# Optimization experiments

Measured on AMD Instinct MI355X. Metric: run time of the kernel, lower is better.

## Reference

```python
import jax, jax.numpy as jnp
import numpy as np
from math import sqrt

# Complete K-ary tree: level l has K**l nodes; children of node j at level l
# are nodes j*K .. j*K+K-1 of level l+1. Levels are processed leaves->root.
K = 4
LEVELS = 9
N_NODES = (K ** LEVELS - 1) // (K - 1)  # 87381
X_SIZE = 256
H_SIZE = 256
A_SIZE = 256
N_HEADS = 8
A_K = A_SIZE // N_HEADS


def setup_inputs() -> dict:
    key = jax.random.key(0)
    ks = jax.random.split(key, 20)
    s = 0.02
    d = {
        'x': jax.random.normal(ks[0], (N_NODES, X_SIZE), dtype=jnp.float32),
        'W_iou': jax.random.normal(ks[1], (X_SIZE, 3 * H_SIZE), dtype=jnp.float32) * s,
        'b_iou': jnp.zeros((3 * H_SIZE,), dtype=jnp.float32),
        'W_f': jax.random.normal(ks[2], (X_SIZE, H_SIZE), dtype=jnp.float32) * s,
        'b_f': jnp.zeros((H_SIZE,), dtype=jnp.float32),
        'Wq': jax.random.normal(ks[3], (X_SIZE, A_SIZE), dtype=jnp.float32) * s,
        'bq': jax.random.normal(ks[4], (A_SIZE,), dtype=jnp.float32) * s,
        'Wk': jax.random.normal(ks[5], (H_SIZE, A_SIZE), dtype=jnp.float32) * s,
        'bk': jax.random.normal(ks[6], (A_SIZE,), dtype=jnp.float32) * s,
        'Wv': jax.random.normal(ks[7], (H_SIZE, A_SIZE), dtype=jnp.float32) * s,
        'bv': jax.random.normal(ks[8], (A_SIZE,), dtype=jnp.float32) * s,
        'Wl': jax.random.normal(ks[9], (A_SIZE, A_SIZE), dtype=jnp.float32) * s,
        'bl': jax.random.normal(ks[10], (A_SIZE,), dtype=jnp.float32) * s,
        'Uiou_w': jax.random.normal(ks[11], (A_SIZE, 3 * H_SIZE), dtype=jnp.float32) * s,
        'Uiou_b': jax.random.normal(ks[12], (3 * H_SIZE,), dtype=jnp.float32) * s,
        'Uf_w': jax.random.normal(ks[13], (A_SIZE, H_SIZE), dtype=jnp.float32) * s,
        'Uf_b': jax.random.normal(ks[14], (H_SIZE,), dtype=jnp.float32) * s,
    }
    return d


def _tree_lstm(x, W_iou, b_iou, W_f, b_f, Wq, bq, Wk, bk, Wv, bv, Wl, bl,
               Uiou_w, Uiou_b, Uf_w, Uf_b):
    scale = 1.0 / sqrt(A_K)
    x_iou = x @ W_iou + b_iou          # [N, 3H]
    x_f = x @ W_f + b_f                # [N, H]
    starts = [(K ** l - 1) // (K - 1) for l in range(LEVELS)]
    h_lvl = [None] * LEVELS
    c_lvl = [None] * LEVELS
    for l in reversed(range(LEVELS)):
        s0 = starts[l]
        n = K ** l
        xi = x_iou[s0:s0 + n]
        xf = x_f[s0:s0 + n]
        if l == LEVELS - 1:  # leaves: empty mailbox
            iou = xi
            fc_sum = jnp.zeros((n, H_SIZE), dtype=x.dtype)
        else:
            ch_h = h_lvl[l + 1].reshape(n, K, H_SIZE)  # children mailbox 'h'
            ch_c = c_lvl[l + 1].reshape(n, K, H_SIZE)  # children mailbox 'c'
            q = (x[s0:s0 + n] @ Wq + bq).reshape(n, N_HEADS, A_K)
            kk = (ch_h @ Wk + bk).reshape(n, K, N_HEADS, A_K)
            vv = (ch_h @ Wv + bv).reshape(n, K, N_HEADS, A_K)
            logits = jnp.einsum('nhd,nkhd->nhk', q, kk) * scale
            attn = jax.nn.softmax(logits, axis=-1)
            out = jnp.einsum('nhk,nkhd->nhd', attn, vv).reshape(n, A_SIZE)
            h_attn = out @ Wl + bl
            h_iou = h_attn @ Uiou_w + Uiou_b
            h_f = h_attn @ Uf_w + Uf_b
            f = jax.nn.sigmoid(xf + h_f)[:, None, :]   # same f for all children
            fc_sum = jnp.sum(ch_c * f, axis=1)
            iou = xi + h_iou
        i, o, u = jnp.split(iou, 3, axis=1)
        c_new = jax.nn.sigmoid(i) * jnp.tanh(u) + fc_sum
        h_new = jax.nn.sigmoid(o) * jnp.tanh(c_new)
        h_lvl[l] = h_new
        c_lvl[l] = c_new
    h = jnp.concatenate(h_lvl, axis=0)
    c = jnp.concatenate(c_lvl, axis=0)
    return h, c


def reference(x, W_iou, b_iou, W_f, b_f, Wq, bq, Wk, bk, Wv, bv, Wl, bl,
              Uiou_w, Uiou_b, Uf_w, Uf_b):
    return _tree_lstm(x, W_iou, b_iou, W_f, b_f, Wq, bq, Wk, bk, Wv, bv,
                      Wl, bl, Uiou_w, Uiou_b, Uf_w, Uf_b)
```

## Files before the change

### kernel.cpp

```cpp
#include <hip/hip_runtime.h>
#include <hip/hip_bf16.h>
#include <math.h>

constexpr int LEVELS_ = 9;
constexpr int N_NODES_ = 87381;
constexpr int HS = 256;
constexpr int N_HEADS_ = 8;

typedef __attribute__((ext_vector_type(8))) short bf16x8;
typedef __attribute__((ext_vector_type(4))) float f32x4;
typedef __attribute__((ext_vector_type(4))) float float4v;

__device__ __forceinline__ short f2bf(float f) {
    union { float f; unsigned u; } a; a.f = f;
    unsigned r = (a.u + 0x7fff + ((a.u >> 16) & 1)) >> 16;
    return (short)r;
}
__device__ __forceinline__ float bf2f(short s) {
    union { unsigned u; float f; } a; a.u = ((unsigned)(unsigned short)s) << 16;
    return a.f;
}
__device__ __forceinline__ float sigm(float x) { return 1.f / (1.f + expf(-x)); }

__device__ __forceinline__ void gl_lds16(const short* g, short* l) {
    __builtin_amdgcn_global_load_lds(
        (const __attribute__((address_space(1))) void*)g,
        (__attribute__((address_space(3))) void*)l, 16, 0, 0);
}

__global__ __launch_bounds__(256) void gemm_bf16(
    const short* __restrict__ A, const short* __restrict__ Bt,
    const float* __restrict__ bias, const short* __restrict__ Cadd,
    void* __restrict__ Cout, int M, int N, int Kd, int out_bf16)
{
    __shared__ short smem[2 * 128 * 64];
    short* As = smem;
    short* Bs = smem + 128 * 64;

    const int tid = threadIdx.x;
    const int lane = tid & 63;
    const int w = tid >> 6;
    const int row0 = blockIdx.y * 128;
    const int col0 = blockIdx.x * 128;
    const int wm = (w >> 1) * 64;
    const int wn = (w & 1) * 64;
    const int q = lane >> 4;
    const int mr = lane & 15;

    const int srl = lane >> 3;
    const int scs = ((lane & 7) ^ srl) * 8;

    f32x4 acc[4][4];
    #pragma unroll
    for (int i = 0; i < 4; i++)
        #pragma unroll
        for (int j = 0; j < 4; j++) acc[i][j] = (f32x4){0.f, 0.f, 0.f, 0.f};

    for (int k0 = 0; k0 < Kd; k0 += 64) {
        __syncthreads();
        #pragma unroll
        for (int i = 0; i < 4; ++i) {
            int s = w * 4 + i;
            int r = s * 8 + srl;
            gl_lds16(A + (size_t)(row0 + r) * Kd + k0 + scs, As + s * 512);
            gl_lds16(Bt + (size_t)(col0 + r) * Kd + k0 + scs, Bs + s * 512);
        }
        __syncthreads();
        #pragma unroll
        for (int h = 0; h < 2; ++h) {
            bf16x8 af[4], bfr[4];
            #pragma unroll
            for (int i = 0; i < 4; ++i) {
                int r = wm + i * 16 + mr;
                af[i] = *(const bf16x8*)(As + r * 64 + ((h * 4 + q) ^ (mr & 7)) * 8);
            }
            #pragma unroll
            for (int j = 0; j < 4; ++j) {
                int r = wn + j * 16 + mr;
                bfr[j] = *(const bf16x8*)(Bs + r * 64 + ((h * 4 + q) ^ (mr & 7)) * 8);
            }
            #pragma unroll
            for (int i = 0; i < 4; ++i)
                #pragma unroll
                for (int j = 0; j < 4; ++j)
                    acc[i][j] = __builtin_amdgcn_mfma_f32_16x16x32_bf16(
                        af[i], bfr[j], acc[i][j], 0, 0, 0);
        }
    }

    if (out_bf16) {
        __syncthreads();
        short* Cs = smem;
        #pragma unroll
        for (int j = 0; j < 4; ++j) {
            int col = wn + j * 16 + mr;
            float bv = bias ? bias[col0 + col] : 0.f;
            #pragma unroll
            for (int i = 0; i < 4; ++i) {
                #pragma unroll
                for (int r = 0; r < 4; ++r) {
                    int lr = wm + i * 16 + q * 4 + r;
                    float v = acc[i][j][r] + bv;
                    if (Cadd && row0 + lr < M)
                        v += bf2f(Cadd[(size_t)(row0 + lr) * N + col0 + col]);
                    Cs[lr * 128 + col] = f2bf(v);
                }
            }
        }
        __syncthreads();
        #pragma unroll
        for (int i = 0; i < 8; ++i) {
            int chunk = i * 256 + tid;
            int lr = chunk >> 4;
            int c8 = (chunk & 15) * 8;
            if (row0 + lr < M)
                *(bf16x8*)((short*)Cout + (size_t)(row0 + lr) * N + col0 + c8) =
                    *(const bf16x8*)(Cs + lr * 128 + c8);
        }
    } else {
        #pragma unroll
        for (int j = 0; j < 4; ++j) {
            int col = col0 + wn + j * 16 + mr;
            float bv = bias ? bias[col] : 0.f;
            #pragma unroll
            for (int i = 0; i < 4; ++i) {
                #pragma unroll
                for (int r = 0; r < 4; ++r) {
                    int grow = row0 + wm + i * 16 + q * 4 + r;
                    if (grow < M) {
                        size_t off = (size_t)grow * N + col;
                        float v = acc[i][j][r] + bv;
                        if (Cadd) v += bf2f(Cadd[off]);
                        ((float*)Cout)[off] = v;
                    }
                }
            }
        }
    }
}

__global__ __launch_bounds__(256) void attn_kernel(
    const short* __restrict__ Q, const short* __restrict__ KV,
    short* __restrict__ Ob, int n)
{
    int t = blockIdx.x * 256 + threadIdx.x;
    int pair = t >> 5;
    int lane = t & 31;
    if (pair >= n * N_HEADS_) return;
    int node = pair >> 3;
    int head = pair & 7;
    const float scale = 0.17677669529663687f;

    int qoff = node * HS + head * 32 + lane;
    float qv = bf2f(Q[qoff]);

    float logit[4];
    #pragma unroll
    for (int c = 0; c < 4; c++) {
        float p = qv * bf2f(KV[(size_t)(4 * node + c) * 512 + head * 32 + lane]);
        #pragma unroll
        for (int off = 16; off >= 1; off >>= 1)
            p += __shfl_xor(p, off, 32);
        logit[c] = p * scale;
    }
    float m = fmaxf(fmaxf(logit[0], logit[1]), fmaxf(logit[2], logit[3]));
    float e[4], s = 0.f;
    #pragma unroll
    for (int c = 0; c < 4; c++) { e[c] = expf(logit[c] - m); s += e[c]; }
    float inv = 1.f / s;
    float o = 0.f;
    #pragma unroll
    for (int c = 0; c < 4; c++)
        o += (e[c] * inv) * bf2f(KV[(size_t)(4 * node + c) * 512 + 256 + head * 32 + lane]);
    Ob[qoff] = f2bf(o);
}

__global__ __launch_bounds__(256) void cell_internal(
    const short* __restrict__ iouf, const float* __restrict__ c_child,
    float* __restrict__ h_out, float* __restrict__ c_out,
    short* __restrict__ hb_out, int n)
{
    int t = blockIdx.x * 256 + threadIdx.x;
    if (t >= n * 32) return;
    int node = t >> 5;
    int j8 = (t & 31) * 8;
    size_t base = (size_t)node * 1024;
    bf16x8 vi = *(const bf16x8*)(iouf + base + j8);
    bf16x8 vo = *(const bf16x8*)(iouf + base + 256 + j8);
    bf16x8 vu = *(const bf16x8*)(iouf + base + 512 + j8);
    bf16x8 vf = *(const bf16x8*)(iouf + base + 768 + j8);
    float4v cc[4][2];
    #pragma unroll
    for (int c = 0; c < 4; ++c) {
        const float* cp = c_child + (size_t)(4 * node + c) * 256 + j8;
        cc[c][0] = *(const float4v*)cp;
        cc[c][1] = *(const float4v*)(cp + 4);
    }
    float4v hv[2], cv[2];
    bf16x8 hbv;
    #pragma unroll
    for (int e = 0; e < 8; ++e) {
        float fv = sigm(bf2f(vf[e]));
        float csum = cc[0][e >> 2][e & 3] + cc[1][e >> 2][e & 3] +
                     cc[2][e >> 2][e & 3] + cc[3][e >> 2][e & 3];
        float cn = sigm(bf2f(vi[e])) * tanhf(bf2f(vu[e])) + csum * fv;
        float hn = sigm(bf2f(vo[e])) * tanhf(cn);
        hv[e >> 2][e & 3] = hn;
        cv[e >> 2][e & 3] = cn;
        hbv[e] = f2bf(hn);
    }
    size_t o = (size_t)t * 8;
    *(float4v*)(h_out + o) = hv[0]; *(float4v*)(h_out + o + 4) = hv[1];
    *(float4v*)(c_out + o) = cv[0]; *(float4v*)(c_out + o + 4) = cv[1];
    *(bf16x8*)(hb_out + o) = hbv;
}

__global__ __launch_bounds__(256) void cell_leaf(
    const short* __restrict__ iou,
    float* __restrict__ h_out, float* __restrict__ c_out,
    short* __restrict__ hb_out, int n)
{
    int t = blockIdx.x * 256 + threadIdx.x;
    if (t >= n * 32) return;
    int node = t >> 5;
    int j8 = (t & 31) * 8;
    size_t base = (size_t)node * 768;
    bf16x8 vi = *(const bf16x8*)(iou + base + j8);
    bf16x8 vo = *(const bf16x8*)(iou + base + 256 + j8);
    bf16x8 vu = *(const bf16x8*)(iou + base + 512 + j8);
    float4v hv[2], cv[2];
    bf16x8 hbv;
    #pragma unroll
    for (int e = 0; e < 8; ++e) {
        float cn = sigm(bf2f(vi[e])) * tanhf(bf2f(vu[e]));
        float hn = sigm(bf2f(vo[e])) * tanhf(cn);
        hv[e >> 2][e & 3] = hn;
        cv[e >> 2][e & 3] = cn;
        hbv[e] = f2bf(hn);
    }
    size_t o = (size_t)t * 8;
    *(float4v*)(h_out + o) = hv[0]; *(float4v*)(h_out + o + 4) = hv[1];
    *(float4v*)(c_out + o) = cv[0]; *(float4v*)(c_out + o + 4) = cv[1];
    *(bf16x8*)(hb_out + o) = hbv;
}

__global__ __launch_bounds__(256) void level_fused(
    const short* __restrict__ hb, const float* __restrict__ c_all,
    const short* __restrict__ qb, const short* __restrict__ xi,
    const short* __restrict__ B3t, const short* __restrict__ Wlt,
    const short* __restrict__ Bt2,
    const float* __restrict__ bias_kv, const float* __restrict__ bl,
    const float* __restrict__ biasU,
    float* __restrict__ h_all, float* __restrict__ c_out_g,
    short* __restrict__ hb_out, int s0, int sc, int n)
{
    __shared__ __align__(16) char smem[50176];
    short* sh_h    = (short*)smem;
    short* sh_kv   = (short*)(smem + 16896);
    short* sh_out  = (short*)smem;
    short* sh_ha   = (short*)(smem + 8448);
    float* sh_iouf = (float*)(smem + 16896);

    const int tid = threadIdx.x;
    const int lane = tid & 63;
    const int w = tid >> 6;
    const int q = lane >> 4;
    const int mr = lane & 15;
    const int p0 = blockIdx.x * 8;
    const int np = (n - p0 < 8) ? (n - p0) : 8;
    const int nch = 4 * np;

    #pragma unroll
    for (int i = 0; i < 4; ++i) {
        int chunk = i * 256 + tid;
        int r = chunk >> 5;
        int c8 = (chunk & 31) * 8;
        bf16x8 v = {};
        if (r < nch) v = *(const bf16x8*)(hb + (size_t)(sc + 4 * p0 + r) * 256 + c8);
        *(bf16x8*)(sh_h + r * 264 + c8) = v;
    }
    __syncthreads();

    {
        f32x4 acc[2][8];
        #pragma unroll
        for (int rt = 0; rt < 2; ++rt)
            #pragma unroll
            for (int ct = 0; ct < 8; ++ct) acc[rt][ct] = (f32x4){0.f, 0.f, 0.f, 0.f};
        #pragma unroll 1
        for (int k0 = 0; k0 < 256; k0 += 32) {
            bf16x8 a0 = *(const bf16x8*)(sh_h + mr * 264 + k0 + q * 8);
            bf16x8 a1 = *(const bf16x8*)(sh_h + (16 + mr) * 264 + k0 + q * 8);
            #pragma unroll
            for (int ct = 0; ct < 8; ++ct) {
                int col = w * 128 + ct * 16 + mr;
                bf16x8 b = *(const bf16x8*)(B3t + (size_t)col * 256 + k0 + q * 8);
                acc[0][ct] = __builtin_amdgcn_mfma_f32_16x16x32_bf16(a0, b, acc[0][ct], 0, 0, 0);
                acc[1][ct] = __builtin_amdgcn_mfma_f32_16x16x32_bf16(a1, b, acc[1][ct], 0, 0, 0);
            }
        }
        #pragma unroll
        for (int ct = 0; ct < 8; ++ct) {
            int col = w * 128 + ct * 16 + mr;
            float bv = bias_kv[col];
            #pragma unroll
            for (int rt = 0; rt < 2; ++rt)
                #pragma unroll
                for (int r = 0; r < 4; ++r) {
                    int row = rt * 16 + q * 4 + r;
                    sh_kv[row * 520 + col] = f2bf(acc[rt][ct][r] + bv);
                }
        }
    }
    __syncthreads();

    {
        const int grp0 = tid >> 5;
        const int l32 = tid & 31;
        #pragma unroll 1
        for (int it = 0; it < 8; ++it) {
            int grp = it * 8 + grp0;
            int node = grp >> 3, head = grp & 7;
            if (node < np) {
                float qv = bf2f(qb[(size_t)(s0 + p0 + node) * 256 + head * 32 + l32]);
                float logit[4];
                #pragma unroll
                for (int c = 0; c < 4; ++c) {
                    float p = qv * bf2f(sh_kv[(4 * node + c) * 520 + head * 32 + l32]);
                    #pragma unroll
                    for (int off = 16; off >= 1; off >>= 1)
                        p += __shfl_xor(p, off, 32);
                    logit[c] = p * 0.17677669529663687f;
                }
                float mx = fmaxf(fmaxf(logit[0], logit[1]), fmaxf(logit[2], logit[3]));
                float e[4], s = 0.f;
                #pragma unroll
                for (int c = 0; c < 4; ++c) { e[c] = expf(logit[c] - mx); s += e[c]; }
                float inv = 1.f / s;
                float o = 0.f;
                #pragma unroll
                for (int c = 0; c < 4; ++c)
                    o += (e[c] * inv) * bf2f(sh_kv[(4 * node + c) * 520 + 256 + head * 32 + l32]);
                sh_out[node * 264 + head * 32 + l32] = f2bf(o);
            }
        }
    }
    __syncthreads();

    {
        f32x4 acc[4];
        #pragma unroll
        for (int ct = 0; ct < 4; ++ct) acc[ct] = (f32x4){0.f, 0.f, 0.f, 0.f};
        #pragma unroll 1
        for (int k0 = 0; k0 < 256; k0 += 32) {
            bf16x8 a = *(const bf16x8*)(sh_out + mr * 264 + k0 + q * 8);
            #pragma unroll
            for (int ct = 0; ct < 4; ++ct) {
                int col = w * 64 + ct * 16 + mr;
                bf16x8 b = *(const bf16x8*)(Wlt + (size_t)col * 256 + k0 + q * 8);
                acc[ct] = __builtin_amdgcn_mfma_f32_16x16x32_bf16(a, b, acc[ct], 0, 0, 0);
            }
        }
        #pragma unroll
        for (int ct = 0; ct < 4; ++ct) {
            int col = w * 64 + ct * 16 + mr;
            float bv = bl[col];
            #pragma unroll
            for (int r = 0; r < 4; ++r) {
                int row = q * 4 + r;
                if (row < np) sh_ha[row * 264 + col] = f2bf(acc[ct][r] + bv);
            }
        }
    }
    __syncthreads();

    {
        f32x4 acc[16];
        #pragma unroll
        for (int ct = 0; ct < 16; ++ct) acc[ct] = (f32x4){0.f, 0.f, 0.f, 0.f};
        #pragma unroll 1
        for (int k0 = 0; k0 < 256; k0 += 32) {
            bf16x8 a = *(const bf16x8*)(sh_ha + mr * 264 + k0 + q * 8);
            #pragma unroll
            for (int ct = 0; ct < 16; ++ct) {
                int col = w * 256 + ct * 16 + mr;
                bf16x8 b = *(const bf16x8*)(Bt2 + (size_t)col * 256 + k0 + q * 8);
                acc[ct] = __builtin_amdgcn_mfma_f32_16x16x32_bf16(a, b, acc[ct], 0, 0, 0);
            }
        }
        __syncthreads();
        #pragma unroll
        for (int ct = 0; ct < 16; ++ct) {
            int col = w * 256 + ct * 16 + mr;
            float bU = biasU[col];
            #pragma unroll
            for (int r = 0; r < 4; ++r) {
                int row = q * 4 + r;
                if (row < np)
                    sh_iouf[row * 1024 + col] =
                        acc[ct][r] + bU + bf2f(xi[(size_t)(s0 + p0 + row) * 1024 + col]);
            }
        }
    }
    __syncthreads();

    #pragma unroll 1
    for (int it = 0; it < 8; ++it) {
        int t = it * 256 + tid;
        if (t < np * 256) {
            int node = t >> 8, j = t & 255;
            float iv = sh_iouf[node * 1024 + j];
            float ov = sh_iouf[node * 1024 + 256 + j];
            float uv = sh_iouf[node * 1024 + 512 + j];
            float fv = sigm(sh_iouf[node * 1024 + 768 + j]);
            float fc = 0.f;
            #pragma unroll
            for (int c = 0; c < 4; ++c)
                fc += c_all[(size_t)(sc + 4 * (p0 + node) + c) * 256 + j] * fv;
            float cn = sigm(iv) * tanhf(uv) + fc;
            float hn = sigm(ov) * tanhf(cn);
            size_t o = (size_t)(s0 + p0 + node) * 256 + j;
            h_all[o] = hn;
            c_out_g[o] = cn;
            hb_out[o] = f2bf(hn);
        }
    }
}

__global__ __launch_bounds__(256) void conv_x(
    const float* __restrict__ x, short* __restrict__ xb, int n8)
{
    int t = blockIdx.x * 256 + threadIdx.x;
    if (t >= n8) return;
    float4v a = *(const float4v*)(x + (size_t)t * 8);
    float4v b = *(const float4v*)(x + (size_t)t * 8 + 4);
    bf16x8 o;
    o[0] = f2bf(a.x); o[1] = f2bf(a.y); o[2] = f2bf(a.z); o[3] = f2bf(a.w);
    o[4] = f2bf(b.x); o[5] = f2bf(b.y); o[6] = f2bf(b.z); o[7] = f2bf(b.w);
    *(bf16x8*)(xb + (size_t)t * 8) = o;
}

__global__ __launch_bounds__(256) void prep_weights(
    const float* __restrict__ W_iou, const float* __restrict__ W_f,
    const float* __restrict__ Uiou_w, const float* __restrict__ Uf_w,
    const float* __restrict__ Wk, const float* __restrict__ Wv,
    const float* __restrict__ Wq, const float* __restrict__ Wl,
    const float* __restrict__ b_iou, const float* __restrict__ b_f,
    const float* __restrict__ Uiou_b, const float* __restrict__ Uf_b,
    const float* __restrict__ bk, const float* __restrict__ bv,
    short* __restrict__ Bt1, short* __restrict__ Bt2, short* __restrict__ B3t,
    short* __restrict__ Wqt, short* __restrict__ Wlt,
    float* __restrict__ biasX, float* __restrict__ biasU,
    float* __restrict__ bias_kv)
{
    int t = blockIdx.x * 256 + threadIdx.x;
    if (t < 262144) {
        int nn = t >> 8, k = t & 255;
        float v = (nn < 768) ? W_iou[k * 768 + nn] : W_f[k * 256 + (nn - 768)];
        Bt1[t] = f2bf(v);
        return;
    }
    t -= 262144;
    if (t < 262144) {
        int nn = t >> 8, k = t & 255;
        float v = (nn < 768) ? Uiou_w[k * 768 + nn] : Uf_w[k * 256 + (nn - 768)];
        Bt2[t] = f2bf(v);
        return;
    }
    t -= 262144;
    if (t < 131072) {
        int nn = t >> 8, k = t & 255;
        float v = (nn < 256) ? Wk[k * 256 + nn] : Wv[k * 256 + (nn - 256)];
        B3t[t] = f2bf(v);
        return;
    }
    t -= 131072;
    if (t < 65536) { int nn = t >> 8, k = t & 255; Wqt[t] = f2bf(Wq[k * 256 + nn]); return; }
    t -= 65536;
    if (t < 65536) { int nn = t >> 8, k = t & 255; Wlt[t] = f2bf(Wl[k * 256 + nn]); return; }
    t -= 65536;
    if (t < 1024) { biasX[t] = (t < 768) ? b_iou[t] : b_f[t - 768]; return; }
    t -= 1024;
    if (t < 1024) { biasU[t] = (t < 768) ? Uiou_b[t] : Uf_b[t - 768]; return; }
    t -= 1024;
    if (t < 512) { bias_kv[t] = (t < 256) ? bk[t] : bv[t - 256]; return; }
}

static inline void launch_gemm(const short* A, const short* Bt, const float* bias,
                               const short* Cadd, void* C, int M, int N, int Kd,
                               int out_bf16, hipStream_t stream)
{
    dim3 grid(N / 128, (M + 127) / 128);
    gemm_bf16<<<grid, 256, 0, stream>>>(A, Bt, bias, Cadd, C, M, N, Kd, out_bf16);
}

extern "C" void kernel_launch(void* const* d_in, const int* in_sizes, int n_in,
                              void* d_out, int out_size, void* d_ws, size_t ws_size,
                              hipStream_t stream)
{
    const float* x      = (const float*)d_in[0];
    const float* W_iou  = (const float*)d_in[1];
    const float* b_iou  = (const float*)d_in[2];
    const float* W_f    = (const float*)d_in[3];
    const float* b_f    = (const float*)d_in[4];
    const float* Wq     = (const float*)d_in[5];
    const float* bq     = (const float*)d_in[6];
    const float* Wk     = (const float*)d_in[7];
    const float* bk     = (const float*)d_in[8];
    const float* Wv     = (const float*)d_in[9];
    const float* bv     = (const float*)d_in[10];
    const float* Wl     = (const float*)d_in[11];
    const float* bl     = (const float*)d_in[12];
    const float* Uiou_w = (const float*)d_in[13];
    const float* Uiou_b = (const float*)d_in[14];
    const float* Uf_w   = (const float*)d_in[15];
    const float* Uf_b   = (const float*)d_in[16];

    float* h_all = (float*)d_out;
    float* c_all = h_all + (size_t)N_NODES_ * HS;

    char* p = (char*)d_ws;
    short* xb   = (short*)p; p += (size_t)N_NODES_ * 256 * 2;
    short* hb   = (short*)p; p += (size_t)N_NODES_ * 256 * 2;
    short* xl   = (short*)p; p += (size_t)65536 * 768 * 2;
    short* xi   = (short*)p; p += (size_t)21845 * 1024 * 2;
    short* qb   = (short*)p; p += (size_t)21845 * 256 * 2;
    short* KVb  = (short*)p; p += (size_t)65536 * 512 * 2;
    short* outb = (short*)p; p += (size_t)16384 * 256 * 2;
    short* hab  = (short*)p; p += (size_t)16384 * 256 * 2;
    short* ioufb= (short*)p; p += (size_t)16384 * 1024 * 2;
    short* Bt1  = (short*)p; p += (size_t)1024 * 256 * 2;
    short* Bt2  = (short*)p; p += (size_t)1024 * 256 * 2;
    short* B3t  = (short*)p; p += (size_t)512 * 256 * 2;
    short* Wqt  = (short*)p; p += (size_t)256 * 256 * 2;
    short* Wlt  = (short*)p; p += (size_t)256 * 256 * 2;
    float* biasX   = (float*)p; p += 1024 * 4;
    float* biasU   = (float*)p; p += 1024 * 4;
    float* bias_kv = (float*)p; p += 512 * 4;

    static const int starts[LEVELS_] = {0, 1, 5, 21, 85, 341, 1365, 5461, 21845};

    {
        int n8 = N_NODES_ * 256 / 8;
        conv_x<<<(n8 + 255) / 256, 256, 0, stream>>>(x, xb, n8);
        int total = 262144 + 262144 + 131072 + 65536 + 65536 + 1024 + 1024 + 512;
        prep_weights<<<(total + 255) / 256, 256, 0, stream>>>(
            W_iou, W_f, Uiou_w, Uf_w, Wk, Wv, Wq, Wl,
            b_iou, b_f, Uiou_b, Uf_b, bk, bv,
            Bt1, Bt2, B3t, Wqt, Wlt, biasX, biasU, bias_kv);
    }

    launch_gemm(xb + (size_t)21845 * 256, Bt1, biasX, nullptr, xl,
                65536, 768, 256, 1, stream);
    launch_gemm(xb, Bt1, biasX, nullptr, xi, 21845, 1024, 256, 1, stream);
    launch_gemm(xb, Wqt, bq, nullptr, qb, 21845, 256, 256, 1, stream);

    {
        int total = 65536 * 32;
        cell_leaf<<<(total + 255) / 256, 256, 0, stream>>>(
            xl, h_all + (size_t)21845 * HS, c_all + (size_t)21845 * HS,
            hb + (size_t)21845 * HS, 65536);
    }

    for (int l = 7; l >= 6; l--) {
        int n  = 1 << (2 * l);
        int s0 = starts[l];
        int sc = starts[l + 1];
        int nc = 4 * n;

        launch_gemm(hb + (size_t)sc * 256, B3t, bias_kv, nullptr, KVb,
                    nc, 512, 256, 1, stream);
        int pairs = n * N_HEADS_;
        attn_kernel<<<(pairs * 32 + 255) / 256, 256, 0, stream>>>(
            qb + (size_t)s0 * 256, KVb, outb, n);
        launch_gemm(outb, Wlt, bl, nullptr, hab, n, 256, 256, 1, stream);
        launch_gemm(hab, Bt2, biasU, xi + (size_t)s0 * 1024, ioufb,
                    n, 1024, 256, 1, stream);
        int total = n * 32;
        cell_internal<<<(total + 255) / 256, 256, 0, stream>>>(
            ioufb, c_all + (size_t)sc * HS,
            h_all + (size_t)s0 * HS, c_all + (size_t)s0 * HS,
            hb + (size_t)s0 * HS, n);
    }

    for (int l = 5; l >= 0; l--) {
        int n  = 1 << (2 * l);
        int s0 = starts[l];
        int sc = starts[l + 1];
        int blocks = (n + 7) / 8;
        level_fused<<<blocks, 256, 0, stream>>>(
            hb, c_all, qb, xi, B3t, Wlt, Bt2, bias_kv, bl, biasU,
            h_all, c_all, hb, s0, sc, n);
    }
}
```

Before: 935.0 us.

## Fuse LSTM cell into gate GEMM epilogues and KV projection with attention

Weight columns are reordered so that each 128-wide GEMM tile holds the i/o/u/f gates for 32 hidden units, and K/V are interleaved per head. That lets the leaf and internal-level GEMMs apply the LSTM cell in their epilogue, and lets the KV projection kernel run the per-head attention directly from shared memory. The large intermediate buffers (leaf iou, KV, iouf) and their round trips through global memory are removed, along with several kernel launches. In exchange the code adds LDS staging and epilogue work, and the level_fused indexing must agree with the new interleaved layout.

```diff
diff --git a/kernel.cpp b/kernel.cpp
--- a/kernel.cpp
+++ b/kernel.cpp
@@ -27,13 +27,14 @@
         (const __attribute__((address_space(1))) void*)g,
         (__attribute__((address_space(3))) void*)l, 16, 0, 0);
 }
+
 
 __global__ __launch_bounds__(256) void gemm_bf16(
     const short* __restrict__ A, const short* __restrict__ Bt,
     const float* __restrict__ bias, const short* __restrict__ Cadd,
     void* __restrict__ Cout, int M, int N, int Kd, int out_bf16)
 {
-    __shared__ short smem[2 * 128 * 64];
+    __shared__ __align__(16) short smem[2 * 128 * 64];
     short* As = smem;
     short* Bs = smem + 128 * 64;
 
@@ -139,109 +140,246 @@
     }
 }
 
-__global__ __launch_bounds__(256) void attn_kernel(
-    const short* __restrict__ Q, const short* __restrict__ KV,
-    short* __restrict__ Ob, int n)
+__global__ __launch_bounds__(256) void gemm_cell(
+    const short* __restrict__ A, const short* __restrict__ Bt,
+    const float* __restrict__ bias, const short* __restrict__ Cadd,
+    const float* __restrict__ c_child,
+    float* __restrict__ h_out, float* __restrict__ c_out,
+    short* __restrict__ hb_out, int M)
 {
-    int t = blockIdx.x * 256 + threadIdx.x;
-    int pair = t >> 5;
-    int lane = t & 31;
-    if (pair >= n * N_HEADS_) return;
-    int node = pair >> 3;
-    int head = pair & 7;
-    const float scale = 0.17677669529663687f;
-
-    int qoff = node * HS + head * 32 + lane;
-    float qv = bf2f(Q[qoff]);
-
-    float logit[4];
+    __shared__ __align__(16) short smem[128 * 136];
+    short* As = smem;
+    short* Bs = smem + 128 * 64;
+
+    const int tid = threadIdx.x;
+    const int lane = tid & 63;
+    const int w = tid >> 6;
+    const int row0 = blockIdx.y * 128;
+    const int col0 = blockIdx.x * 128;
+    const int wm = (w >> 1) * 64;
+    const int wn = (w & 1) * 64;
+    const int q = lane >> 4;
+    const int mr = lane & 15;
+
+    const int srl = lane >> 3;
+    const int scs = ((lane & 7) ^ srl) * 8;
+
+    f32x4 acc[4][4];
     #pragma unroll
-    for (int c = 0; c < 4; c++) {
-        float p = qv * bf2f(KV[(size_t)(4 * node + c) * 512 + head * 32 + lane]);
-        #pragma unroll
-        for (int off = 16; off >= 1; off >>= 1)
-            p += __shfl_xor(p, off, 32);
-        logit[c] = p * scale;
-    }
-    float m = fmaxf(fmaxf(logit[0], logit[1]), fmaxf(logit[2], logit[3]));
-    float e[4], s = 0.f;
+    for (int i = 0; i < 4; i++)
+        #pragma unroll
+        for (int j = 0; j < 4; j++) acc[i][j] = (f32x4){0.f, 0.f, 0.f, 0.f};
+
+    for (int k0 = 0; k0 < 256; k0 += 64) {
+        __syncthreads();
+        #pragma unroll
+        for (int i = 0; i < 4; ++i) {
+            int s = w * 4 + i;
+            int r = s * 8 + srl;
+            gl_lds16(A + (size_t)(row0 + r) * 256 + k0 + scs, As + s * 512);
+            gl_lds16(Bt + (size_t)(col0 + r) * 256 + k0 + scs, Bs + s * 512);
+        }
+        __syncthreads();
+        #pragma unroll
+        for (int h = 0; h < 2; ++h) {
+            bf16x8 af[4], bfr[4];
+            #pragma unroll
+            for (int i = 0; i < 4; ++i) {
+                int r = wm + i * 16 + mr;
+                af[i] = *(const bf16x8*)(As + r * 64 + ((h * 4 + q) ^ (mr & 7)) * 8);
+            }
+            #pragma unroll
+            for (int j = 0; j < 4; ++j) {
+                int r = wn + j * 16 + mr;
+                bfr[j] = *(const bf16x8*)(Bs + r * 64 + ((h * 4 + q) ^ (mr & 7)) * 8);
+            }
+            #pragma unroll
+            for (int i = 0; i < 4; ++i)
+                #pragma unroll
+                for (int j = 0; j < 4; ++j)
+                    acc[i][j] = __builtin_amdgcn_mfma_f32_16x16x32_bf16(
+                        af[i], bfr[j], acc[i][j], 0, 0, 0);
+        }
+    }
+
+    __syncthreads();
+    short* Cs = smem;
     #pragma unroll
-    for (int c = 0; c < 4; c++) { e[c] = expf(logit[c] - m); s += e[c]; }
-    float inv = 1.f / s;
-    float o = 0.f;
+    for (int j = 0; j < 4; ++j) {
+        int col = wn + j * 16 + mr;
+        float bv = bias[col0 + col];
+        #pragma unroll
+        for (int i = 0; i < 4; ++i) {
+            #pragma unroll
+            for (int r = 0; r < 4; ++r) {
+                int lr = wm + i * 16 + q * 4 + r;
+                float v = acc[i][j][r] + bv;
+                if (Cadd && row0 + lr < M)
+                    v += bf2f(Cadd[(size_t)(row0 + lr) * 1024 + col0 + col]);
+                Cs[lr * 136 + col] = f2bf(v);
+            }
+        }
+    }
+    __syncthreads();
+
+    const int hd0 = blockIdx.x * 32;
+    #pragma unroll 1
+    for (int it = 0; it < 2; ++it) {
+        int chunk = it * 256 + tid;
+        int row = chunk >> 2;
+        int d8 = (chunk & 3) * 8;
+        int gp = row0 + row;
+        if (gp < M) {
+            bf16x8 vi = *(const bf16x8*)(Cs + row * 136 + d8);
+            bf16x8 vo = *(const bf16x8*)(Cs + row * 136 + 32 + d8);
+            bf16x8 vu = *(const bf16x8*)(Cs + row * 136 + 64 + d8);
+            float fc[8] = {0.f, 0.f, 0.f, 0.f, 0.f, 0.f, 0.f, 0.f};
+            if (c_child) {
+                bf16x8 vf = *(const bf16x8*)(Cs + row * 136 + 96 + d8);
+                #pragma unroll
+                for (int c = 0; c < 4; ++c) {
+                    const float* cp = c_child + (size_t)(4 * gp + c) * 256 + hd0 + d8;
+                    float4v a = *(const float4v*)cp;
+                    float4v b = *(const float4v*)(cp + 4);
+                    #pragma unroll
+                    for (int e = 0; e < 4; ++e) { fc[e] += a[e]; fc[4 + e] += b[e]; }
+                }
+                #pragma unroll
+                for (int e = 0; e < 8; ++e) fc[e] *= sigm(bf2f(vf[e]));
+            }
+            float4v hv[2], cv[2];
+            bf16x8 hbv;
+            #pragma unroll
+            for (int e = 0; e < 8; ++e) {
+                float cn = sigm(bf2f(vi[e])) * tanhf(bf2f(vu[e])) + fc[e];
+                float hn = sigm(bf2f(vo[e])) * tanhf(cn);
+                hv[e >> 2][e & 3] = hn;
+                cv[e >> 2][e & 3] = cn;
+                hbv[e] = f2bf(hn);
+            }
+            size_t o = (size_t)gp * 256 + hd0 + d8;
+            *(float4v*)(h_out + o) = hv[0]; *(float4v*)(h_out + o + 4) = hv[1];
+            *(float4v*)(c_out + o) = cv[0]; *(float4v*)(c_out + o + 4) = cv[1];
+            *(bf16x8*)(hb_out + o) = hbv;
+        }
+    }
+}
+
+__global__ __launch_bounds__(256) void kv_attn(
+    const short* __restrict__ A,
+    const short* __restrict__ B3t,
+    const float* __restrict__ bias_kv,
+    const short* __restrict__ qb_lvl,
+    short* __restrict__ outb)
+{
+    __shared__ __align__(16) short smem[2 * 128 * 64 + 32 * 64];
+    short* As = smem;
+    short* Bs = smem + 128 * 64;
+    short* sh_o = smem + 2 * 128 * 64;
+
+    const int tid = threadIdx.x;
+    const int lane = tid & 63;
+    const int w = tid >> 6;
+    const int row0 = blockIdx.y * 128;
+    const int colb = blockIdx.x;
+    const int col0 = colb * 128;
+    const int wm = (w >> 1) * 64;
+    const int wn = (w & 1) * 64;
+    const int q = lane >> 4;
+    const int mr = lane & 15;
+
+    const int srl = lane >> 3;
+    const int scs = ((lane & 7) ^ srl) * 8;
+
+    f32x4 acc[4][4];
     #pragma unroll
-    for (int c = 0; c < 4; c++)
-        o += (e[c] * inv) * bf2f(KV[(size_t)(4 * node + c) * 512 + 256 + head * 32 + lane]);
-    Ob[qoff] = f2bf(o);
-}
-
-__global__ __launch_bounds__(256) void cell_internal(
-    const short* __restrict__ iouf, const float* __restrict__ c_child,
-    float* __restrict__ h_out, float* __restrict__ c_out,
-    short* __restrict__ hb_out, int n)
-{
-    int t = blockIdx.x * 256 + threadIdx.x;
-    if (t >= n * 32) return;
-    int node = t >> 5;
-    int j8 = (t & 31) * 8;
-    size_t base = (size_t)node * 1024;
-    bf16x8 vi = *(const bf16x8*)(iouf + base + j8);
-    bf16x8 vo = *(const bf16x8*)(iouf + base + 256 + j8);
-    bf16x8 vu = *(const bf16x8*)(iouf + base + 512 + j8);
-    bf16x8 vf = *(const bf16x8*)(iouf + base + 768 + j8);
-    float4v cc[4][2];
+    for (int i = 0; i < 4; i++)
+        #pragma unroll
+        for (int j = 0; j < 4; j++) acc[i][j] = (f32x4){0.f, 0.f, 0.f, 0.f};
+
+    for (int k0 = 0; k0 < 256; k0 += 64) {
+        __syncthreads();
+        #pragma unroll
+        for (int i = 0; i < 4; ++i) {
+            int s = w * 4 + i;
+            int r = s * 8 + srl;
+            gl_lds16(A + (size_t)(row0 + r) * 256 + k0 + scs, As + s * 512);
+            gl_lds16(B3t + (size_t)(col0 + r) * 256 + k0 + scs, Bs + s * 512);
+        }
+        __syncthreads();
+        #pragma unroll
+        for (int h = 0; h < 2; ++h) {
+            bf16x8 af[4], bfr[4];
+            #pragma unroll
+            for (int i = 0; i < 4; ++i) {
+                int r = wm + i * 16 + mr;
+                af[i] = *(const bf16x8*)(As + r * 64 + ((h * 4 + q) ^ (mr & 7)) * 8);
+            }
+            #pragma unroll
+            for (int j = 0; j < 4; ++j) {
+                int r = wn + j * 16 + mr;
+                bfr[j] = *(const bf16x8*)(Bs + r * 64 + ((h * 4 + q) ^ (mr & 7)) * 8);
+            }
+            #pragma unroll
+            for (int i = 0; i < 4; ++i)
+                #pragma unroll
+                for (int j = 0; j < 4; ++j)
+                    acc[i][j] = __builtin_amdgcn_mfma_f32_16x16x32_bf16(
+                        af[i], bfr[j], acc[i][j], 0, 0, 0);
+        }
+    }
+
+    __syncthreads();
+    short* Cs = smem;
     #pragma unroll
-    for (int c = 0; c < 4; ++c) {
-        const float* cp = c_child + (size_t)(4 * node + c) * 256 + j8;
-        cc[c][0] = *(const float4v*)cp;
-        cc[c][1] = *(const float4v*)(cp + 4);
-    }
-    float4v hv[2], cv[2];
-    bf16x8 hbv;
-    #pragma unroll
-    for (int e = 0; e < 8; ++e) {
-        float fv = sigm(bf2f(vf[e]));
-        float csum = cc[0][e >> 2][e & 3] + cc[1][e >> 2][e & 3] +
-                     cc[2][e >> 2][e & 3] + cc[3][e >> 2][e & 3];
-        float cn = sigm(bf2f(vi[e])) * tanhf(bf2f(vu[e])) + csum * fv;
-        float hn = sigm(bf2f(vo[e])) * tanhf(cn);
-        hv[e >> 2][e & 3] = hn;
-        cv[e >> 2][e & 3] = cn;
-        hbv[e] = f2bf(hn);
-    }
-    size_t o = (size_t)t * 8;
-    *(float4v*)(h_out + o) = hv[0]; *(float4v*)(h_out + o + 4) = hv[1];
-    *(float4v*)(c_out + o) = cv[0]; *(float4v*)(c_out + o + 4) = cv[1];
-    *(bf16x8*)(hb_out + o) = hbv;
-}
-
-__global__ __launch_bounds__(256) void cell_leaf(
-    const short* __restrict__ iou,
-    float* __restrict__ h_out, float* __restrict__ c_out,
-    short* __restrict__ hb_out, int n)
-{
-    int t = blockIdx.x * 256 + threadIdx.x;
-    if (t >= n * 32) return;
-    int node = t >> 5;
-    int j8 = (t & 31) * 8;
-    size_t base = (size_t)node * 768;
-    bf16x8 vi = *(const bf16x8*)(iou + base + j8);
-    bf16x8 vo = *(const bf16x8*)(iou + base + 256 + j8);
-    bf16x8 vu = *(const bf16x8*)(iou + base + 512 + j8);
-    float4v hv[2], cv[2];
-    bf16x8 hbv;
-    #pragma unroll
-    for (int e = 0; e < 8; ++e) {
-        float cn = sigm(bf2f(vi[e])) * tanhf(bf2f(vu[e]));
-        float hn = sigm(bf2f(vo[e])) * tanhf(cn);
-        hv[e >> 2][e & 3] = hn;
-        cv[e >> 2][e & 3] = cn;
-        hbv[e] = f2bf(hn);
-    }
-    size_t o = (size_t)t * 8;
-    *(float4v*)(h_out + o) = hv[0]; *(float4v*)(h_out + o + 4) = hv[1];
-    *(float4v*)(c_out + o) = cv[0]; *(float4v*)(c_out + o + 4) = cv[1];
-    *(bf16x8*)(hb_out + o) = hbv;
+    for (int j = 0; j < 4; ++j) {
+        int col = wn + j * 16 + mr;
+        float bv = bias_kv[col0 + col];
+        #pragma unroll
+        for (int i = 0; i < 4; ++i) {
+            #pragma unroll
+            for (int r = 0; r < 4; ++r) {
+                int lr = wm + i * 16 + q * 4 + r;
+                Cs[lr * 128 + col] = f2bf(acc[i][j][r] + bv);
+            }
+        }
+    }
+    __syncthreads();
+
+    const int p0 = blockIdx.y * 32;
+    const int grp0 = tid >> 5;
+    const int l32 = tid & 31;
+    #pragma unroll 1
+    for (int it = 0; it < 8; ++it) {
+        int pair = it * 8 + grp0;
+        int pl = pair >> 1, hh = pair & 1;
+        float qv = bf2f(qb_lvl[(size_t)(p0 + pl) * 256 + (colb * 2 + hh) * 32 + l32]);
+        float logit[4];
+        #pragma unroll
+        for (int c = 0; c < 4; ++c) {
+            float pch = qv * bf2f(Cs[(4 * pl + c) * 128 + hh * 64 + l32]);
+            #pragma unroll
+            for (int off = 16; off >= 1; off >>= 1)
+                pch += __shfl_xor(pch, off, 32);
+            logit[c] = pch * 0.17677669529663687f;
+        }
+        float mx = fmaxf(fmaxf(logit[0], logit[1]), fmaxf(logit[2], logit[3]));
+        float e[4], s = 0.f;
+        #pragma unroll
+        for (int c = 0; c < 4; ++c) { e[c] = expf(logit[c] - mx); s += e[c]; }
+        float inv = 1.f / s;
+        float o = 0.f;
+        #pragma unroll
+        for (int c = 0; c < 4; ++c)
+            o += (e[c] * inv) * bf2f(Cs[(4 * pl + c) * 128 + hh * 64 + 32 + l32]);
+        sh_o[pl * 64 + hh * 32 + l32] = f2bf(o);
+    }
+    __syncthreads();
+    {
+        int r = tid >> 3, c8 = (tid & 7) * 8;
+        *(bf16x8*)(outb + (size_t)(p0 + r) * 256 + colb * 64 + c8) =
+            *(const bf16x8*)(sh_o + r * 64 + c8);
+    }
 }
 
 __global__ __launch_bounds__(256) void level_fused(
@@ -326,7 +464,7 @@
                 float logit[4];
                 #pragma unroll
                 for (int c = 0; c < 4; ++c) {
-                    float p = qv * bf2f(sh_kv[(4 * node + c) * 520 + head * 32 + l32]);
+                    float p = qv * bf2f(sh_kv[(4 * node + c) * 520 + head * 64 + l32]);
                     #pragma unroll
                     for (int off = 16; off >= 1; off >>= 1)
                         p += __shfl_xor(p, off, 32);
@@ -340,7 +478,7 @@
                 float o = 0.f;
                 #pragma unroll
                 for (int c = 0; c < 4; ++c)
-                    o += (e[c] * inv) * bf2f(sh_kv[(4 * node + c) * 520 + 256 + head * 32 + l32]);
+                    o += (e[c] * inv) * bf2f(sh_kv[(4 * node + c) * 520 + head * 64 + 32 + l32]);
                 sh_out[node * 264 + head * 32 + l32] = f2bf(o);
             }
         }
@@ -409,10 +547,11 @@
         int t = it * 256 + tid;
         if (t < np * 256) {
             int node = t >> 8, j = t & 255;
-            float iv = sh_iouf[node * 1024 + j];
-            float ov = sh_iouf[node * 1024 + 256 + j];
-            float uv = sh_iouf[node * 1024 + 512 + j];
-            float fv = sigm(sh_iouf[node * 1024 + 768 + j]);
+            int gcol = (j >> 5) * 128 + (j & 31);
+            float iv = sh_iouf[node * 1024 + gcol];
+            float ov = sh_iouf[node * 1024 + gcol + 32];
+            float uv = sh_iouf[node * 1024 + gcol + 64];
+            float fv = sigm(sh_iouf[node * 1024 + gcol + 96]);
             float fc = 0.f;
             #pragma unroll
             for (int c = 0; c < 4; ++c)
@@ -455,22 +594,25 @@
 {
     int t = blockIdx.x * 256 + threadIdx.x;
     if (t < 262144) {
-        int nn = t >> 8, k = t & 255;
-        float v = (nn < 768) ? W_iou[k * 768 + nn] : W_f[k * 256 + (nn - 768)];
+        int gc = t >> 8, k = t & 255;
+        int within = gc & 127, gate = within >> 5, d = (gc >> 7) * 32 + (within & 31);
+        float v = (gate < 3) ? W_iou[k * 768 + gate * 256 + d] : W_f[k * 256 + d];
         Bt1[t] = f2bf(v);
         return;
     }
     t -= 262144;
     if (t < 262144) {
-        int nn = t >> 8, k = t & 255;
-        float v = (nn < 768) ? Uiou_w[k * 768 + nn] : Uf_w[k * 256 + (nn - 768)];
+        int gc = t >> 8, k = t & 255;
+        int within = gc & 127, gate = within >> 5, d = (gc >> 7) * 32 + (within & 31);
+        float v = (gate < 3) ? Uiou_w[k * 768 + gate * 256 + d] : Uf_w[k * 256 + d];
         Bt2[t] = f2bf(v);
         return;
     }
     t -= 262144;
     if (t < 131072) {
-        int nn = t >> 8, k = t & 255;
-        float v = (nn < 256) ? Wk[k * 256 + nn] : Wv[k * 256 + (nn - 256)];
+        int gc = t >> 8, k = t & 255;
+        int head = gc >> 6, kv = (gc >> 5) & 1, d = head * 32 + (gc & 31);
+        float v = kv ? Wv[k * 256 + d] : Wk[k * 256 + d];
         B3t[t] = f2bf(v);
         return;
     }
@@ -479,11 +621,23 @@
     t -= 65536;
     if (t < 65536) { int nn = t >> 8, k = t & 255; Wlt[t] = f2bf(Wl[k * 256 + nn]); return; }
     t -= 65536;
-    if (t < 1024) { biasX[t] = (t < 768) ? b_iou[t] : b_f[t - 768]; return; }
+    if (t < 1024) {
+        int within = t & 127, gate = within >> 5, d = (t >> 7) * 32 + (within & 31);
+        biasX[t] = (gate < 3) ? b_iou[gate * 256 + d] : b_f[d];
+        return;
+    }
     t -= 1024;
-    if (t < 1024) { biasU[t] = (t < 768) ? Uiou_b[t] : Uf_b[t - 768]; return; }
+    if (t < 1024) {
+        int within = t & 127, gate = within >> 5, d = (t >> 7) * 32 + (within & 31);
+        biasU[t] = (gate < 3) ? Uiou_b[gate * 256 + d] : Uf_b[d];
+        return;
+    }
     t -= 1024;
-    if (t < 512) { bias_kv[t] = (t < 256) ? bk[t] : bv[t - 256]; return; }
+    if (t < 512) {
+        int head = t >> 6, kv = (t >> 5) & 1, d = head * 32 + (t & 31);
+        bias_kv[t] = kv ? bv[d] : bk[d];
+        return;
+    }
 }
 
 static inline void launch_gemm(const short* A, const short* Bt, const float* bias,
@@ -522,13 +676,10 @@
     char* p = (char*)d_ws;
     short* xb   = (short*)p; p += (size_t)N_NODES_ * 256 * 2;
     short* hb   = (short*)p; p += (size_t)N_NODES_ * 256 * 2;
-    short* xl   = (short*)p; p += (size_t)65536 * 768 * 2;
     short* xi   = (short*)p; p += (size_t)21845 * 1024 * 2;
     short* qb   = (short*)p; p += (size_t)21845 * 256 * 2;
-    short* KVb  = (short*)p; p += (size_t)65536 * 512 * 2;
     short* outb = (short*)p; p += (size_t)16384 * 256 * 2;
     short* hab  = (short*)p; p += (size_t)16384 * 256 * 2;
-    short* ioufb= (short*)p; p += (size_t)16384 * 1024 * 2;
     short* Bt1  = (short*)p; p += (size_t)1024 * 256 * 2;
     short* Bt2  = (short*)p; p += (size_t)1024 * 256 * 2;
     short* B3t  = (short*)p; p += (size_t)512 * 256 * 2;
@@ -550,15 +701,14 @@
             Bt1, Bt2, B3t, Wqt, Wlt, biasX, biasU, bias_kv);
     }
 
-    launch_gemm(xb + (size_t)21845 * 256, Bt1, biasX, nullptr, xl,
-                65536, 768, 256, 1, stream);
     launch_gemm(xb, Bt1, biasX, nullptr, xi, 21845, 1024, 256, 1, stream);
     launch_gemm(xb, Wqt, bq, nullptr, qb, 21845, 256, 256, 1, stream);
 
     {
-        int total = 65536 * 32;
-        cell_leaf<<<(total + 255) / 256, 256, 0, stream>>>(
-            xl, h_all + (size_t)21845 * HS, c_all + (size_t)21845 * HS,
+        dim3 grid(8, 65536 / 128);
+        gemm_cell<<<grid, 256, 0, stream>>>(
+            xb + (size_t)21845 * 256, Bt1, biasX, nullptr, nullptr,
+            h_all + (size_t)21845 * HS, c_all + (size_t)21845 * HS,
             hb + (size_t)21845 * HS, 65536);
     }
 
@@ -568,17 +718,13 @@
         int sc = starts[l + 1];
         int nc = 4 * n;
 
-        launch_gemm(hb + (size_t)sc * 256, B3t, bias_kv, nullptr, KVb,
-                    nc, 512, 256, 1, stream);
-        int pairs = n * N_HEADS_;
-        attn_kernel<<<(pairs * 32 + 255) / 256, 256, 0, stream>>>(
-            qb + (size_t)s0 * 256, KVb, outb, n);
+        dim3 gkv(4, nc / 128);
+        kv_attn<<<gkv, 256, 0, stream>>>(
+            hb + (size_t)sc * 256, B3t, bias_kv, qb + (size_t)s0 * 256, outb);
         launch_gemm(outb, Wlt, bl, nullptr, hab, n, 256, 256, 1, stream);
-        launch_gemm(hab, Bt2, biasU, xi + (size_t)s0 * 1024, ioufb,
-                    n, 1024, 256, 1, stream);
-        int total = n * 32;
-        cell_internal<<<(total + 255) / 256, 256, 0, stream>>>(
-            ioufb, c_all + (size_t)sc * HS,
+        dim3 gc(8, n / 128);
+        gemm_cell<<<gc, 256, 0, stream>>>(
+            hab, Bt2, biasU, xi + (size_t)s0 * 1024, c_all + (size_t)sc * HS,
             h_all + (size_t)s0 * HS, c_all + (size_t)s0 * HS,
             hb + (size_t)s0 * HS, n);
     }
```

Result: faster. 880.3 us (-5.9%).
